# Performance work log

Hardware: AMD Instinct MI355X
Metric: run time of the kernel (lower is better)

The kernel has to match this reference:

```python
import jax, jax.numpy as jnp
import numpy as np
import math

HEADS = 8

def setup_inputs() -> dict:
    key = jax.random.key(0)
    k1, k2 = jax.random.split(key)
    B, C, H, W = 8, 512, 32, 32
    x = jax.random.normal(k1, (B, C, H, W), dtype=jnp.float32)
    # weight-norm 1x1 conv params: v ~ N(0, 0.05), g initialized to ||v|| (torch weight_norm default)
    proj_v = jax.random.normal(k2, (3 * C, C), dtype=jnp.float32) * 0.05
    proj_g = jnp.linalg.norm(proj_v, axis=1)
    proj_b = jnp.zeros((3 * C,), dtype=jnp.float32)
    return {"x": x, "proj_v": proj_v, "proj_g": proj_g, "proj_b": proj_b}

def reference(x, proj_v, proj_g, proj_b):
    B, C, H, W = x.shape
    heads = HEADS
    dim = C // heads
    N = H * W
    # weight-normalized 1x1 conv: w = g * v / ||v|| per output channel
    w = proj_g[:, None] * proj_v / jnp.linalg.norm(proj_v, axis=1, keepdims=True)
    c = jnp.einsum('oc,bchw->bohw', w, x) + proj_b[None, :, None, None]
    c = c.reshape(B, 3, heads, dim, N)
    q, k, v = c[:, 0], c[:, 1], c[:, 2]  # each (B, heads, dim, N)
    scale = 1.0 / math.sqrt(dim)
    attn = jnp.einsum('bhdq,bhdk->bhqk', q, k) * scale  # (B, heads, N, N)
    attn = jax.nn.softmax(attn, axis=-1)
    out = jnp.einsum('bhdk,bhqk->bhdq', v, attn)  # (B, heads, dim, N)
    return x + out.reshape(B, C, H, W)
```

## Files before the change

kernel.cpp:

```cpp
#include <hip/hip_runtime.h>

typedef _Float16 f16;
typedef _Float16 f16x2 __attribute__((ext_vector_type(2)));
typedef _Float16 f16x4 __attribute__((ext_vector_type(4)));
typedef _Float16 f16x8 __attribute__((ext_vector_type(8)));
typedef float f32x4 __attribute__((ext_vector_type(4)));
typedef float f32x16 __attribute__((ext_vector_type(16)));
typedef unsigned int u32;
typedef unsigned int u32x4 __attribute__((ext_vector_type(4)));

__device__ inline f32x16 mfma32(f16x8 a, f16x8 b, f32x16 c) {
    return __builtin_amdgcn_mfma_f32_32x32x16_f16(a, b, c, 0, 0, 0);
}

__device__ inline u32 pk2u(float a, float b) {
    return __builtin_bit_cast(u32, __builtin_amdgcn_cvt_pkrtz(a, b));
}

__device__ inline void gl16(const f16* g, f16* l) {
    __builtin_amdgcn_global_load_lds(
        (const __attribute__((address_space(1))) void*)g,
        (__attribute__((address_space(3))) void*)l, 16, 0, 0);
}

__global__ __launch_bounds__(256) void prep_k(const float* __restrict__ pv,
                                              const float* __restrict__ pg,
                                              f16* __restrict__ w,
                                              const float* __restrict__ x,
                                              f16* __restrict__ xT) {
    int bid = blockIdx.x;
    if (bid < 1536) {
        int o = bid;
        const float* row = pv + (size_t)o * 512;
        float s = 0.f;
        for (int c = threadIdx.x; c < 512; c += 256) { float t = row[c]; s += t * t; }
        for (int off = 32; off; off >>= 1) s += __shfl_down(s, off, 64);
        __shared__ float red[4];
        int lane = threadIdx.x & 63, wid = threadIdx.x >> 6;
        if (lane == 0) red[wid] = s;
        __syncthreads();
        float tot = red[0] + red[1] + red[2] + red[3];
        float scale = pg[o] * rsqrtf(tot);
        for (int c = threadIdx.x; c < 512; c += 256)
            w[(size_t)o * 512 + c] = (f16)(row[c] * scale);
    } else {
        int t2 = bid - 1536;
        int n0 = (t2 & 31) * 32, c0 = ((t2 >> 5) & 15) * 32, b = t2 >> 9;
        int tx = threadIdx.x & 31, ty = threadIdx.x >> 5;
        __shared__ float t[32][33];
        const float* xb = x + (size_t)b * 512 * 1024;
        for (int i = 0; i < 4; i++)
            t[ty + 8 * i][tx] = xb[(size_t)(c0 + ty + 8 * i) * 1024 + n0 + tx];
        __syncthreads();
        f16* xTb = xT + (size_t)b * 1024 * 512;
        for (int i = 0; i < 4; i++)
            xTb[(size_t)(n0 + ty + 8 * i) * 512 + c0 + tx] = (f16)t[tx][ty + 8 * i];
    }
}

__global__ __launch_bounds__(256) void qkv_gemm_k(const f16* __restrict__ w,
                                                  const f16* __restrict__ xT,
                                                  const float* __restrict__ pb,
                                                  f16* __restrict__ qk,
                                                  f16* __restrict__ v) {
    __shared__ f16 lA[128 * 64];
    __shared__ f16 lB[128 * 64];
    int b = blockIdx.z;
    int oBase = blockIdx.y * 128;
    int nBase = blockIdx.x * 128;
    const f16* xb = xT + (size_t)b * 1024 * 512;
    int tid = threadIdx.x, lane = tid & 63, warp = tid >> 6;
    int wy = warp >> 1, wx = warp & 1;
    int l31 = lane & 31, hi = lane >> 5;

    int srow = lane >> 3;
    int phys = lane & 7;
    int schunk = phys ^ srow;
    const f16* aS[4]; const f16* bS[4]; f16* dA[4]; f16* dB[4];
    for (int j = 0; j < 4; j++) {
        int rb = (warp * 4 + j) * 8;
        aS[j] = w  + (size_t)(oBase + rb + srow) * 512 + schunk * 8;
        bS[j] = xb + (size_t)(nBase + rb + srow) * 512 + schunk * 8;
        dA[j] = &lA[rb * 64];
        dB[j] = &lB[rb * 64];
    }
    int phk[4];
    for (int ks = 0; ks < 4; ks++)
        phk[ks] = (((ks * 2 + hi) ^ (l31 & 7))) * 8;

    f32x16 acc[2][2] = {};

    for (int i = 0; i < 8; i++) {
        int k0 = i * 64;
        __syncthreads();
        for (int j = 0; j < 4; j++) {
            gl16(aS[j] + k0, dA[j]);
            gl16(bS[j] + k0, dB[j]);
        }
        __syncthreads();
        for (int ks = 0; ks < 4; ks++) {
            f16x8 af[2], bf[2];
            for (int mi = 0; mi < 2; mi++)
                af[mi] = *(f16x8*)&lA[(wy * 64 + mi * 32 + l31) * 64 + phk[ks]];
            for (int ni = 0; ni < 2; ni++)
                bf[ni] = *(f16x8*)&lB[(wx * 64 + ni * 32 + l31) * 64 + phk[ks]];
            for (int mi = 0; mi < 2; mi++)
                for (int ni = 0; ni < 2; ni++)
                    acc[mi][ni] = mfma32(af[mi], bf[ni], acc[mi][ni]);
        }
    }

    int selB = oBase >> 9;
    for (int mi = 0; mi < 2; mi++) {
        for (int g = 0; g < 4; g++) {
            int oR = oBase + wy * 64 + mi * 32 + 8 * g + 4 * hi;
            int h = (oR >> 6) & 7, d0 = oR & 63;
            for (int ni = 0; ni < 2; ni++) {
                int n = nBase + wx * 64 + ni * 32 + l31;
                if (selB < 2) {
                    float sc = selB == 0 ? 0.125f : 1.0f;
                    f16x4 o4;
                    for (int r = 0; r < 4; r++)
                        o4[r] = (f16)((acc[mi][ni][g * 4 + r] + pb[oR + r]) * sc);
                    *(f16x4*)&qk[((((size_t)b * 2 + selB) * 8 + h) * 1024 + n) * 64 + d0] = o4;
                } else {
                    for (int r = 0; r < 4; r++) {
                        float val = acc[mi][ni][g * 4 + r] + pb[oR + r];
                        v[(((size_t)b * 8 + h) * 64 + d0 + r) * 1024 + n] = (f16)val;
                    }
                }
            }
        }
    }
}

#define TSZ 4096

__global__ __launch_bounds__(256, 2) void attn_k(const f16* __restrict__ qk,
                                                 const f16* __restrict__ vg,
                                                 const float* __restrict__ x,
                                                 float* __restrict__ out) {
    __shared__ __align__(16) f16 smem[4 * TSZ];
    int bh = blockIdx.y;
    int b = bh >> 3, h = bh & 7;
    int qBase = blockIdx.x * 128;
    int tid = threadIdx.x, lane = tid & 63, warp = tid >> 6;
    int l31 = lane & 31, hi = lane >> 5;

    const f16* qbase = qk + (((size_t)b * 2 + 0) * 8 + h) * 1024 * 64;
    const f16* kbase = qk + (((size_t)b * 2 + 1) * 8 + h) * 1024 * 64;
    const f16* vbase = vg + ((size_t)b * 8 + h) * 64 * 1024;

    int q0 = qBase + warp * 32;
    f16x8 aq[4];
    for (int ks = 0; ks < 4; ks++)
        aq[ks] = *(const f16x8*)&qbase[(size_t)(q0 + l31) * 64 + ks * 16 + hi * 8];

    int rb = lane >> 3;
    int gchunk = (lane & 7) ^ rb;
    const f16* kS0 = kbase + (size_t)(warp * 8 + rb) * 64 + gchunk * 8;
    const f16* vS0 = vbase + (size_t)(warp * 8 + rb) * 1024 + gchunk * 8;

    f32x16 accO[2] = {};
    float l_acc = 0.f;

#define STAGE(BUF, KT)                                                        \
    do {                                                                      \
        f16* lb = smem + (BUF) * 2 * TSZ;                                     \
        const f16* ks_ = kS0 + (size_t)(KT) * 4096;                           \
        const f16* vs_ = vS0 + (size_t)(KT) * 64;                             \
        gl16(ks_,             lb + warp * 512);                               \
        gl16(ks_ + 32 * 64,   lb + 2048 + warp * 512);                        \
        gl16(vs_,             lb + TSZ + warp * 512);                         \
        gl16(vs_ + 32 * 1024, lb + TSZ + 2048 + warp * 512);                  \
    } while (0)

    STAGE(0, 0);
    __syncthreads();

    for (int kt = 0; kt < 16; kt++) {
        int cur = kt & 1;
        if (kt < 15) STAGE(cur ^ 1, kt + 1);
        const f16* lK = smem + cur * 2 * TSZ;
        const f16* lV = lK + TSZ;

        u32 P0[2][4], P1[2][4];
        float rs = 0.f;
        for (int mt = 0; mt < 2; mt++) {
            f16x8 ak[4];
            for (int ks = 0; ks < 4; ks++) {
                int row = mt * 32 + l31;
                ak[ks] = *(const f16x8*)&lK[row * 64 + (((ks * 2 + hi) ^ (l31 & 7)) << 3)];
            }
            f32x16 stt = {};
            for (int ks = 0; ks < 4; ks++)
                stt = mfma32(ak[ks], aq[ks], stt);
            for (int g = 0; g < 4; g++) {
                float p0 = __expf(stt[g * 4 + 0]);
                float p1 = __expf(stt[g * 4 + 1]);
                float p2 = __expf(stt[g * 4 + 2]);
                float p3 = __expf(stt[g * 4 + 3]);
                rs += (p0 + p1) + (p2 + p3);
                P0[mt][g] = pk2u(p0, p1);
                P1[mt][g] = pk2u(p2, p3);
            }
        }
        l_acc += rs;

        f16x8 av[2][4];
        for (int dt = 0; dt < 2; dt++)
            for (int ks = 0; ks < 4; ks++) {
                int row = dt * 32 + l31;
                av[dt][ks] = *(const f16x8*)&lV[row * 64 + (((ks * 2 + hi) ^ (l31 & 7)) << 3)];
            }
        f16x8 bfrag[4];
        for (int ks = 0; ks < 4; ks++) {
            int mt = ks >> 1, ge = 2 * (ks & 1);
            u32 e00 = P0[mt][ge], e01 = P0[mt][ge + 1];
            u32 e10 = P1[mt][ge], e11 = P1[mt][ge + 1];
            u32 k0 = hi ? e01 : e00;
            u32 k1 = hi ? e11 : e10;
            u32 s0 = hi ? e00 : e01;
            u32 s1 = hi ? e10 : e11;
            u32 r0 = __shfl_xor(s0, 32, 64);
            u32 r1 = __shfl_xor(s1, 32, 64);
            u32 a0 = hi ? r0 : k0, a1 = hi ? r1 : k1;
            u32 b0 = hi ? k0 : r0, b1 = hi ? k1 : r1;
            u32x4 t = {a0, a1, b0, b1};
            bfrag[ks] = __builtin_bit_cast(f16x8, t);
        }
        for (int dt = 0; dt < 2; dt++)
            for (int ks = 0; ks < 4; ks++)
                accO[dt] = mfma32(av[dt][ks], bfrag[ks], accO[dt]);

        __syncthreads();
    }
#undef STAGE

    float lt = l_acc + __shfl_xor(l_acc, 32, 64);
    float rl = 1.0f / lt;
    int q = q0 + l31;
    for (int dt = 0; dt < 2; dt++)
        for (int g = 0; g < 4; g++)
            for (int r = 0; r < 4; r++) {
                int d = dt * 32 + 8 * g + 4 * hi + r;
                size_t gi = ((size_t)b * 512 + h * 64 + d) * 1024 + q;
                out[gi] = x[gi] + accO[dt][g * 4 + r] * rl;
            }
}

extern "C" void kernel_launch(void* const* d_in, const int* in_sizes, int n_in,
                              void* d_out, int out_size, void* d_ws, size_t ws_size,
                              hipStream_t stream) {
    (void)in_sizes; (void)n_in; (void)out_size; (void)ws_size;
    const float* x  = (const float*)d_in[0];
    const float* pv = (const float*)d_in[1];
    const float* pg = (const float*)d_in[2];
    const float* pb = (const float*)d_in[3];
    float* out = (float*)d_out;

    char* ws = (char*)d_ws;
    f16* w   = (f16*)(ws);
    f16* xT  = (f16*)(ws + 1572864);
    f16* qk  = (f16*)(ws + 1572864 + 8388608);
    f16* v   = (f16*)(ws + 1572864 + 8388608 + 16777216);

    hipLaunchKernelGGL(prep_k,     dim3(5632),     dim3(256), 0, stream, pv, pg, w, x, xT);
    hipLaunchKernelGGL(qkv_gemm_k, dim3(8, 12, 8), dim3(256), 0, stream, w, xT, pb, qk, v);
    hipLaunchKernelGGL(attn_k,     dim3(8, 64),    dim3(256), 0, stream, qk, v, x, out);
}
```

Measured before the change: 129.0 us.

## Use single-wave attention blocks with 32-key tiles and vmcnt waits instead of barriers

The attention kernel becomes one 64-thread wave per block, each owning 32 queries and streaming 32-key K/V tiles through a double-buffered LDS ring. With only one wave per block, __syncthreads disappears and explicit s_waitcnt vmcnt waits on the async global-to-LDS loads take its place. The grid is reordered so blockIdx.x indexes batch-head. The intent is to remove barrier stalls and raise scheduling flexibility, but each wave now loads the full K/V for its head alone, multiplying global/L2 traffic compared with four waves sharing a tile.

```diff
diff --git a/kernel.cpp b/kernel.cpp
--- a/kernel.cpp
+++ b/kernel.cpp
@@ -134,90 +134,92 @@
     }
 }
 
-#define TSZ 4096
-
-__global__ __launch_bounds__(256, 2) void attn_k(const f16* __restrict__ qk,
-                                                 const f16* __restrict__ vg,
-                                                 const float* __restrict__ x,
-                                                 float* __restrict__ out) {
-    __shared__ __align__(16) f16 smem[4 * TSZ];
-    int bh = blockIdx.y;
+__global__ __launch_bounds__(64, 2) void attn_k(const f16* __restrict__ qk,
+                                                const f16* __restrict__ vg,
+                                                const float* __restrict__ x,
+                                                float* __restrict__ out) {
+    __shared__ __align__(16) f16 smem[8192];
+    int bh = blockIdx.x;
     int b = bh >> 3, h = bh & 7;
-    int qBase = blockIdx.x * 128;
-    int tid = threadIdx.x, lane = tid & 63, warp = tid >> 6;
-    int l31 = lane & 31, hi = lane >> 5;
+    int tid = threadIdx.x;
+    int l31 = tid & 31, hi = tid >> 5;
 
     const f16* qbase = qk + (((size_t)b * 2 + 0) * 8 + h) * 1024 * 64;
     const f16* kbase = qk + (((size_t)b * 2 + 1) * 8 + h) * 1024 * 64;
     const f16* vbase = vg + ((size_t)b * 8 + h) * 64 * 1024;
 
-    int q0 = qBase + warp * 32;
+    int q0 = blockIdx.y * 32;
     f16x8 aq[4];
     for (int ks = 0; ks < 4; ks++)
         aq[ks] = *(const f16x8*)&qbase[(size_t)(q0 + l31) * 64 + ks * 16 + hi * 8];
 
-    int rb = lane >> 3;
-    int gchunk = (lane & 7) ^ rb;
-    const f16* kS0 = kbase + (size_t)(warp * 8 + rb) * 64 + gchunk * 8;
-    const f16* vS0 = vbase + (size_t)(warp * 8 + rb) * 1024 + gchunk * 8;
+    int kr = tid >> 3, kch = (tid & 7) ^ kr;
+    const f16* kS = kbase + (size_t)kr * 64 + kch * 8;
+    int vr = tid >> 2, vch = (tid & 3) ^ (vr & 3);
+    const f16* vS = vbase + (size_t)vr * 1024 + vch * 8;
+
+#define STAGE(BUF, KT)                                                        \
+    do {                                                                      \
+        f16* lbK = smem + (BUF) * 4096;                                       \
+        f16* lbV = lbK + 2048;                                                \
+        const f16* ks_ = kS + (size_t)(KT) * 32 * 64;                         \
+        const f16* vs_ = vS + (size_t)(KT) * 32;                              \
+        gl16(ks_,            lbK);                                            \
+        gl16(ks_ + 8 * 64,   lbK + 512);                                      \
+        gl16(ks_ + 16 * 64,  lbK + 1024);                                     \
+        gl16(ks_ + 24 * 64,  lbK + 1536);                                     \
+        gl16(vs_,              lbV);                                          \
+        gl16(vs_ + 16 * 1024,  lbV + 512);                                    \
+        gl16(vs_ + 32 * 1024,  lbV + 1024);                                   \
+        gl16(vs_ + 48 * 1024,  lbV + 1536);                                   \
+    } while (0)
 
     f32x16 accO[2] = {};
     float l_acc = 0.f;
 
-#define STAGE(BUF, KT)                                                        \
-    do {                                                                      \
-        f16* lb = smem + (BUF) * 2 * TSZ;                                     \
-        const f16* ks_ = kS0 + (size_t)(KT) * 4096;                           \
-        const f16* vs_ = vS0 + (size_t)(KT) * 64;                             \
-        gl16(ks_,             lb + warp * 512);                               \
-        gl16(ks_ + 32 * 64,   lb + 2048 + warp * 512);                        \
-        gl16(vs_,             lb + TSZ + warp * 512);                         \
-        gl16(vs_ + 32 * 1024, lb + TSZ + 2048 + warp * 512);                  \
-    } while (0)
-
     STAGE(0, 0);
-    __syncthreads();
-
-    for (int kt = 0; kt < 16; kt++) {
+
+    for (int kt = 0; kt < 32; kt++) {
         int cur = kt & 1;
-        if (kt < 15) STAGE(cur ^ 1, kt + 1);
-        const f16* lK = smem + cur * 2 * TSZ;
-        const f16* lV = lK + TSZ;
-
-        u32 P0[2][4], P1[2][4];
+        if (kt < 31) {
+            STAGE(cur ^ 1, kt + 1);
+            asm volatile("s_waitcnt vmcnt(8)" ::: "memory");
+        } else {
+            asm volatile("s_waitcnt vmcnt(0)" ::: "memory");
+        }
+        const f16* lK = smem + cur * 4096;
+        const f16* lV = lK + 2048;
+
+        f16x8 ak[4];
+        for (int ks = 0; ks < 4; ks++)
+            ak[ks] = *(const f16x8*)&lK[l31 * 64 + (((ks * 2 + hi) ^ (l31 & 7)) << 3)];
+        f32x16 stt = {};
+        for (int ks = 0; ks < 4; ks++)
+            stt = mfma32(ak[ks], aq[ks], stt);
+        u32 P0[4], P1[4];
         float rs = 0.f;
-        for (int mt = 0; mt < 2; mt++) {
-            f16x8 ak[4];
-            for (int ks = 0; ks < 4; ks++) {
-                int row = mt * 32 + l31;
-                ak[ks] = *(const f16x8*)&lK[row * 64 + (((ks * 2 + hi) ^ (l31 & 7)) << 3)];
+        for (int g = 0; g < 4; g++) {
+            float p0 = __expf(stt[g * 4 + 0]);
+            float p1 = __expf(stt[g * 4 + 1]);
+            float p2 = __expf(stt[g * 4 + 2]);
+            float p3 = __expf(stt[g * 4 + 3]);
+            rs += (p0 + p1) + (p2 + p3);
+            P0[g] = pk2u(p0, p1);
+            P1[g] = pk2u(p2, p3);
+        }
+        l_acc += rs;
+
+        f16x8 av[2][2];
+        for (int dt = 0; dt < 2; dt++)
+            for (int ks2 = 0; ks2 < 2; ks2++) {
+                int row = dt * 32 + l31;
+                av[dt][ks2] = *(const f16x8*)&lV[row * 32 + (((ks2 * 2 + hi) ^ (l31 & 3)) << 3)];
             }
-            f32x16 stt = {};
-            for (int ks = 0; ks < 4; ks++)
-                stt = mfma32(ak[ks], aq[ks], stt);
-            for (int g = 0; g < 4; g++) {
-                float p0 = __expf(stt[g * 4 + 0]);
-                float p1 = __expf(stt[g * 4 + 1]);
-                float p2 = __expf(stt[g * 4 + 2]);
-                float p3 = __expf(stt[g * 4 + 3]);
-                rs += (p0 + p1) + (p2 + p3);
-                P0[mt][g] = pk2u(p0, p1);
-                P1[mt][g] = pk2u(p2, p3);
-            }
-        }
-        l_acc += rs;
-
-        f16x8 av[2][4];
-        for (int dt = 0; dt < 2; dt++)
-            for (int ks = 0; ks < 4; ks++) {
-                int row = dt * 32 + l31;
-                av[dt][ks] = *(const f16x8*)&lV[row * 64 + (((ks * 2 + hi) ^ (l31 & 7)) << 3)];
-            }
-        f16x8 bfrag[4];
-        for (int ks = 0; ks < 4; ks++) {
-            int mt = ks >> 1, ge = 2 * (ks & 1);
-            u32 e00 = P0[mt][ge], e01 = P0[mt][ge + 1];
-            u32 e10 = P1[mt][ge], e11 = P1[mt][ge + 1];
+        f16x8 bfrag[2];
+        for (int ks2 = 0; ks2 < 2; ks2++) {
+            int ge = 2 * ks2;
+            u32 e00 = P0[ge], e01 = P0[ge + 1];
+            u32 e10 = P1[ge], e11 = P1[ge + 1];
             u32 k0 = hi ? e01 : e00;
             u32 k1 = hi ? e11 : e10;
             u32 s0 = hi ? e00 : e01;
@@ -227,13 +229,11 @@
             u32 a0 = hi ? r0 : k0, a1 = hi ? r1 : k1;
             u32 b0 = hi ? k0 : r0, b1 = hi ? k1 : r1;
             u32x4 t = {a0, a1, b0, b1};
-            bfrag[ks] = __builtin_bit_cast(f16x8, t);
+            bfrag[ks2] = __builtin_bit_cast(f16x8, t);
         }
         for (int dt = 0; dt < 2; dt++)
-            for (int ks = 0; ks < 4; ks++)
-                accO[dt] = mfma32(av[dt][ks], bfrag[ks], accO[dt]);
-
-        __syncthreads();
+            for (int ks2 = 0; ks2 < 2; ks2++)
+                accO[dt] = mfma32(av[dt][ks2], bfrag[ks2], accO[dt]);
     }
 #undef STAGE
 
@@ -267,5 +267,5 @@
 
     hipLaunchKernelGGL(prep_k,     dim3(5632),     dim3(256), 0, stream, pv, pg, w, x, xT);
     hipLaunchKernelGGL(qkv_gemm_k, dim3(8, 12, 8), dim3(256), 0, stream, w, xT, pb, qk, v);
-    hipLaunchKernelGGL(attn_k,     dim3(8, 64),    dim3(256), 0, stream, qk, v, x, out);
-}
+    hipLaunchKernelGGL(attn_k,     dim3(64, 32),   dim3(64),  0, stream, qk, v, x, out);
+}
```

Measured after the change: 135.3 us. +4.9%, slower.

## Double-buffer QKV GEMM LDS tiles with prefetch of next K slice

Applied to the files above, without the earlier changes.

Restructures the QKV projection GEMM main loop to use two LDS buffers with K-slices of 32 instead of a single buffer with 64. The next slice is loaded via global_load_lds while the current slice feeds MFMAs, which drops one barrier per iteration and overlaps memory with compute. The XOR swizzle is adapted to the narrower row width. It doubles the iteration count and adds a buffer. Correctness relies on the loads completing at the single remaining barrier.

```diff
diff --git a/kernel.cpp b/kernel.cpp
--- a/kernel.cpp
+++ b/kernel.cpp
@@ -63,8 +63,7 @@
                                                   const float* __restrict__ pb,
                                                   f16* __restrict__ qk,
                                                   f16* __restrict__ v) {
-    __shared__ f16 lA[128 * 64];
-    __shared__ f16 lB[128 * 64];
+    __shared__ f16 smem[4 * 4096];
     int b = blockIdx.z;
     int oBase = blockIdx.y * 128;
     int nBase = blockIdx.x * 128;
@@ -73,42 +72,51 @@
     int wy = warp >> 1, wx = warp & 1;
     int l31 = lane & 31, hi = lane >> 5;
 
-    int srow = lane >> 3;
-    int phys = lane & 7;
-    int schunk = phys ^ srow;
-    const f16* aS[4]; const f16* bS[4]; f16* dA[4]; f16* dB[4];
-    for (int j = 0; j < 4; j++) {
-        int rb = (warp * 4 + j) * 8;
-        aS[j] = w  + (size_t)(oBase + rb + srow) * 512 + schunk * 8;
-        bS[j] = xb + (size_t)(nBase + rb + srow) * 512 + schunk * 8;
-        dA[j] = &lA[rb * 64];
-        dB[j] = &lB[rb * 64];
-    }
-    int phk[4];
-    for (int ks = 0; ks < 4; ks++)
-        phk[ks] = (((ks * 2 + hi) ^ (l31 & 7))) * 8;
+    int srow = lane >> 2;
+    int cg = (lane & 3) ^ (srow & 3);
+    const f16* aS0 = w  + (size_t)(oBase + warp * 32 + srow) * 512 + cg * 8;
+    const f16* aS1 = w  + (size_t)(oBase + warp * 32 + 16 + srow) * 512 + cg * 8;
+    const f16* bS0 = xb + (size_t)(nBase + warp * 32 + srow) * 512 + cg * 8;
+    const f16* bS1 = xb + (size_t)(nBase + warp * 32 + 16 + srow) * 512 + cg * 8;
+
+#define QSTAGE(BUF, IT)                                                       \
+    do {                                                                      \
+        int k0_ = (IT) * 32;                                                  \
+        f16* lAb = smem + (BUF) * 8192;                                       \
+        f16* lBb = lAb + 4096;                                                \
+        gl16(aS0 + k0_, lAb + (warp * 2 + 0) * 512);                          \
+        gl16(aS1 + k0_, lAb + (warp * 2 + 1) * 512);                          \
+        gl16(bS0 + k0_, lBb + (warp * 2 + 0) * 512);                          \
+        gl16(bS1 + k0_, lBb + (warp * 2 + 1) * 512);                          \
+    } while (0)
 
     f32x16 acc[2][2] = {};
 
-    for (int i = 0; i < 8; i++) {
-        int k0 = i * 64;
-        __syncthreads();
-        for (int j = 0; j < 4; j++) {
-            gl16(aS[j] + k0, dA[j]);
-            gl16(bS[j] + k0, dB[j]);
-        }
-        __syncthreads();
-        for (int ks = 0; ks < 4; ks++) {
+    QSTAGE(0, 0);
+    __syncthreads();
+
+    for (int i = 0; i < 16; i++) {
+        int cur = i & 1;
+        if (i < 15) QSTAGE(cur ^ 1, i + 1);
+        const f16* lAc = smem + cur * 8192;
+        const f16* lBc = lAc + 4096;
+        for (int ks = 0; ks < 2; ks++) {
             f16x8 af[2], bf[2];
-            for (int mi = 0; mi < 2; mi++)
-                af[mi] = *(f16x8*)&lA[(wy * 64 + mi * 32 + l31) * 64 + phk[ks]];
-            for (int ni = 0; ni < 2; ni++)
-                bf[ni] = *(f16x8*)&lB[(wx * 64 + ni * 32 + l31) * 64 + phk[ks]];
+            for (int mi = 0; mi < 2; mi++) {
+                int row = wy * 64 + mi * 32 + l31;
+                af[mi] = *(const f16x8*)&lAc[row * 32 + (((ks * 2 + hi) ^ (l31 & 3)) * 8)];
+            }
+            for (int ni = 0; ni < 2; ni++) {
+                int row = wx * 64 + ni * 32 + l31;
+                bf[ni] = *(const f16x8*)&lBc[row * 32 + (((ks * 2 + hi) ^ (l31 & 3)) * 8)];
+            }
             for (int mi = 0; mi < 2; mi++)
                 for (int ni = 0; ni < 2; ni++)
                     acc[mi][ni] = mfma32(af[mi], bf[ni], acc[mi][ni]);
         }
-    }
+        __syncthreads();
+    }
+#undef QSTAGE
 
     int selB = oBase >> 9;
     for (int mi = 0; mi < 2; mi++) {
```

Result: no change. 129.6 us (+0.4%).
